# Performance work log

Hardware: AMD Instinct MI355X
Metric: run time of the kernel (lower is better)

The kernel has to match this reference:

```python
import jax, jax.numpy as jnp
import numpy as np

N = 100000      # nodes
E = 1600000     # edges
NODE_DIM = 128
HID = 128
L = 3           # num_layers
B = 512         # graphs in batch
EPS = 1e-5      # LayerNorm eps


def setup_inputs() -> dict:
    key = jax.random.key(0)
    ks = jax.random.split(key, 8)
    nodes = jax.random.normal(ks[0], (N, NODE_DIM), jnp.float32)
    edges = jax.random.randint(ks[1], (2, E), 0, N, dtype=jnp.int32)
    edge_types = jax.random.randint(ks[2], (E,), 0, 10, dtype=jnp.int32)
    batch_idx = jnp.sort(jax.random.randint(ks[3], (N,), 0, B, dtype=jnp.int32))
    w_in = jax.random.normal(ks[4], (NODE_DIM, HID), jnp.float32) / np.sqrt(NODE_DIM)
    b_in = jnp.zeros((HID,), jnp.float32)
    gcn_w = jax.random.normal(ks[5], (L, HID, HID), jnp.float32) / np.sqrt(HID)
    gcn_b = jnp.zeros((L, HID), jnp.float32)
    ln_g = jnp.ones((L, HID), jnp.float32)
    ln_b = jnp.zeros((L, HID), jnp.float32)
    return {"nodes": nodes, "edges": edges, "edge_types": edge_types,
            "batch_idx": batch_idx, "w_in": w_in, "b_in": b_in,
            "gcn_w": gcn_w, "gcn_b": gcn_b, "ln_g": ln_g, "ln_b": ln_b}


def _layer_norm(x, g, b):
    mu = jnp.mean(x, axis=-1, keepdims=True)
    var = jnp.mean(jnp.square(x - mu), axis=-1, keepdims=True)
    return (x - mu) * jax.lax.rsqrt(var + EPS) * g + b


def reference(nodes, edges, edge_types, batch_idx, w_in, b_in, gcn_w, gcn_b, ln_g, ln_b):
    src, dst = edges[0], edges[1]
    # GCN normalization with self-loops: deg = in-degree(A) + 1
    deg = jax.ops.segment_sum(jnp.ones((E,), nodes.dtype), dst, num_segments=N) + 1.0
    dinv_sqrt = jax.lax.rsqrt(deg)
    dinv = 1.0 / deg                       # self-loop norm = 1/deg_i
    enorm = dinv_sqrt[src] * dinv_sqrt[dst]

    x = nodes @ w_in + b_in                # input projection [N, HID]
    for i in range(L):
        res = x
        xw = x @ gcn_w[i]
        agg = jax.ops.segment_sum(xw[src] * enorm[:, None], dst, num_segments=N)
        x = agg + xw * dinv[:, None] + gcn_b[i]
        x = jax.nn.relu(_layer_norm(x, ln_g[i], ln_b[i]))
        # dropout is identity in eval mode
        if i > 0:
            x = x + res                    # residual only for i > 0

    # global mean pool per graph
    counts = jax.ops.segment_sum(jnp.ones((N,), x.dtype), batch_idx, num_segments=B)
    plan = jax.ops.segment_sum(x, batch_idx, num_segments=B) / jnp.maximum(counts, 1.0)[:, None]
    return x, plan
```

## Files before the change

kernel.cpp:

```cpp
#include <hip/hip_runtime.h>
#include <hip/hip_bf16.h>

typedef __attribute__((ext_vector_type(8))) short bf16x8;
typedef __attribute__((ext_vector_type(4))) float f32x4;
typedef __attribute__((ext_vector_type(2))) float f32x2;

#define K1_TILE 6144
#define NBCAP 4608
#define PAD 136

__device__ __forceinline__ unsigned short f2bf(float f) {
    union { unsigned int i; float f; } x; x.f = f;
    unsigned int r = (x.i + 0x7fffu + ((x.i >> 16) & 1u)) >> 16;
    return (unsigned short)r;
}
__device__ __forceinline__ float blo(unsigned int u) { return __uint_as_float(u << 16); }
__device__ __forceinline__ float bhi(unsigned int u) { return __uint_as_float(u & 0xffff0000u); }


__global__ __launch_bounds__(256) void bin2_k(const int* __restrict__ src,
                                              const int* __restrict__ dst,
                                              int* __restrict__ bucket_cursor,
                                              int* __restrict__ bins,
                                              int E, int NB) {
    __shared__ int hist[512];
    __shared__ int lbase[513];
    __shared__ int gdiff[512];
    __shared__ int wsum[4];
    __shared__ int stage[K1_TILE];
    int tid = threadIdx.x;
    int base = blockIdx.x * K1_TILE;
    int cnt = min(K1_TILE, E - base);

    hist[tid] = 0; hist[tid + 256] = 0;
    __syncthreads();
    for (int i = tid; i < cnt; i += 256) atomicAdd(&hist[dst[base + i] >> 8], 1);
    __syncthreads();

    int h0 = hist[2 * tid], h1 = hist[2 * tid + 1];
    int v = h0 + h1;
    int lane = tid & 63, wid = tid >> 6;
    int s = v;
#pragma unroll
    for (int o = 1; o < 64; o <<= 1) { int n = __shfl_up(s, o); if (lane >= o) s += n; }
    if (lane == 63) wsum[wid] = s;
    __syncthreads();
    if (tid == 0) { int r = 0; for (int w = 0; w < 4; ++w) { int t2 = wsum[w]; wsum[w] = r; r += t2; } }
    __syncthreads();
    int lb0 = s + wsum[wid] - v;
    int lb1 = lb0 + h0;
    int b0 = 2 * tid, b1 = 2 * tid + 1;
    int gb0 = 0, gb1 = 0;
    if (h0 > 0 && b0 < NB) gb0 = atomicAdd(&bucket_cursor[b0], h0);
    if (h1 > 0 && b1 < NB) gb1 = atomicAdd(&bucket_cursor[b1], h1);
    __syncthreads();
    hist[b0] = lb0; hist[b1] = lb1;
    lbase[b0] = lb0; lbase[b1] = lb1;
    gdiff[b0] = gb0 - lb0; gdiff[b1] = gb1 - lb1;
    if (tid == 0) lbase[512] = cnt;
    __syncthreads();

    for (int i = tid; i < cnt; i += 256) {
        int sv = src[base + i], dv = dst[base + i];
        int pos = atomicAdd(&hist[dv >> 8], 1);
        stage[pos] = ((dv & 255) << 24) | sv;
    }
    __syncthreads();

    for (int i = tid; i < cnt; i += 256) {
        int lo = 0, hi = 512;
        while (lo + 1 < hi) { int mid = (lo + hi) >> 1; if (lbase[mid] <= i) lo = mid; else hi = mid; }
        int p = gdiff[lo] + i;
        if (p < NBCAP) bins[(size_t)lo * NBCAP + p] = stage[i];
    }
}


__global__ __launch_bounds__(256) void bucket_scan_k(const int* __restrict__ bucket_cursor,
                                                     int* __restrict__ bucket_base, int NB) {
    __shared__ int wsum[4];
    int tid = threadIdx.x;
    int h0 = (2 * tid < NB) ? min(bucket_cursor[2 * tid], NBCAP) : 0;
    int h1 = (2 * tid + 1 < NB) ? min(bucket_cursor[2 * tid + 1], NBCAP) : 0;
    int v = h0 + h1;
    int lane = tid & 63, wid = tid >> 6;
    int s = v;
#pragma unroll
    for (int o = 1; o < 64; o <<= 1) { int n = __shfl_up(s, o); if (lane >= o) s += n; }
    if (lane == 63) wsum[wid] = s;
    __syncthreads();
    if (tid == 0) { int r = 0; for (int w = 0; w < 4; ++w) { int t2 = wsum[w]; wsum[w] = r; r += t2; } }
    __syncthreads();
    int excl = s + wsum[wid] - v;
    if (2 * tid < NB) bucket_base[2 * tid] = excl;
    if (2 * tid + 1 < NB) bucket_base[2 * tid + 1] = excl + h0;
}


__global__ __launch_bounds__(256) void csr_build_k(const int* __restrict__ bins,
                                                   const int* __restrict__ bucket_cursor,
                                                   const int* __restrict__ bucket_base,
                                                   int* __restrict__ csr_src,
                                                   int* __restrict__ row_start,
                                                   float* __restrict__ dinv_sqrt,
                                                   float* __restrict__ dinv,
                                                   int N) {
    __shared__ int counts[256];
    __shared__ int cursor[256];
    __shared__ int wsum[4];
    __shared__ int lcsr[NBCAP];
    int b = blockIdx.x, tid = threadIdx.x;
    int cnt = min(bucket_cursor[b], NBCAP);
    int cbase = bucket_base[b];
    const int* my = bins + (size_t)b * NBCAP;

    counts[tid] = 0;
    __syncthreads();
    for (int i = tid; i < cnt; i += 256) atomicAdd(&counts[((unsigned)my[i]) >> 24], 1);
    __syncthreads();

    int v = counts[tid];
    int lane = tid & 63, wid = tid >> 6;
    int s = v;
#pragma unroll
    for (int o = 1; o < 64; o <<= 1) { int n = __shfl_up(s, o); if (lane >= o) s += n; }
    if (lane == 63) wsum[wid] = s;
    __syncthreads();
    if (tid == 0) { int r = 0; for (int w = 0; w < 4; ++w) { int t2 = wsum[w]; wsum[w] = r; r += t2; } }
    __syncthreads();
    int excl = s + wsum[wid] - v;

    int node = b * 256 + tid;
    if (node <= N) row_start[node] = cbase + excl;
    if (node < N) {
        float dg = (float)v + 1.0f;
        dinv_sqrt[node] = rsqrtf(dg);
        dinv[node] = 1.0f / dg;
    }
    cursor[tid] = excl;
    __syncthreads();

    for (int i = tid; i < cnt; i += 256) {
        int e = my[i];
        int pos = atomicAdd(&cursor[((unsigned)e) >> 24], 1);
        lcsr[pos] = e & 0xffffff;
    }
    __syncthreads();
    for (int i = tid; i < cnt; i += 256) csr_src[cbase + i] = lcsr[i];
}


__global__ __launch_bounds__(256) void pack_w_k(const float* __restrict__ w_in,
                                                const float* __restrict__ gcn_w,
                                                unsigned short* __restrict__ Wp) {
    int t = blockIdx.x * 256 + threadIdx.x;
    if (t >= 8192) return;
    int mat = t >> 11;
    int kb = (t >> 9) & 3;
    int ct = (t >> 6) & 7;
    int lane = t & 63;
    int q = lane >> 4, c = lane & 15;
    const float* W = (mat == 0) ? w_in : (gcn_w + (size_t)(mat - 1) * 16384);
    unsigned short o[8];
#pragma unroll
    for (int j = 0; j < 8; ++j)
        o[j] = f2bf(W[(size_t)(kb * 32 + q * 8 + j) * 128 + ct * 16 + c]);
    unsigned short* dstp = Wp + ((size_t)t) * 8;
#pragma unroll
    for (int j = 0; j < 8; ++j) dstp[j] = o[j];
}


__global__ __launch_bounds__(256) void proj_k(const float* __restrict__ A,
                                              const unsigned short* __restrict__ Wp,
                                              const float* __restrict__ bias,
                                              unsigned short* __restrict__ Cb,
                                              int M) {
    __shared__ unsigned short stage[64 * 128];
    int wid = threadIdx.x >> 6, lane = threadIdx.x & 63;
    int blk0 = blockIdx.x * 64;
    int r0 = blk0 + wid * 16;
    int q = lane >> 4, c = lane & 15;
    int ar = min(r0 + c, M - 1);

    f32x4 acc[8];
#pragma unroll
    for (int ct = 0; ct < 8; ++ct) acc[ct] = (f32x4){0.f, 0.f, 0.f, 0.f};

#pragma unroll
    for (int kb = 0; kb < 4; ++kb) {
        float4 f0 = *(const float4*)&A[(size_t)ar * 128 + kb * 32 + q * 8];
        float4 f1 = *(const float4*)&A[(size_t)ar * 128 + kb * 32 + q * 8 + 4];
        union { unsigned short u[8]; bf16x8 v; } af;
        af.u[0] = f2bf(f0.x); af.u[1] = f2bf(f0.y); af.u[2] = f2bf(f0.z); af.u[3] = f2bf(f0.w);
        af.u[4] = f2bf(f1.x); af.u[5] = f2bf(f1.y); af.u[6] = f2bf(f1.z); af.u[7] = f2bf(f1.w);
#pragma unroll
        for (int ct = 0; ct < 8; ++ct) {
            bf16x8 b = *(const bf16x8*)&Wp[(((size_t)(kb * 8 + ct)) * 64 + lane) * 8];
            acc[ct] = __builtin_amdgcn_mfma_f32_16x16x32_bf16(af.v, b, acc[ct], 0, 0, 0);
        }
    }

#pragma unroll
    for (int ct = 0; ct < 8; ++ct) {
        int col = ct * 16 + c;
        float bv = bias[col];
#pragma unroll
        for (int r = 0; r < 4; ++r)
            stage[(wid * 16 + q * 4 + r) * 128 + col] = f2bf(acc[ct][r] + bv);
    }
    __syncthreads();

    int tid = threadIdx.x;
#pragma unroll
    for (int i = 0; i < 4; ++i) {
        int k = tid + i * 256;
        int row = k >> 4, colc = (k & 15) * 8;
        int grow = blk0 + row;
        if (grow < M)
            *(uint4*)&Cb[(size_t)grow * 128 + colc] = *(const uint4*)&stage[row * 128 + colc];
    }
}


__device__ __forceinline__ void acc8(f32x2& a0, f32x2& a1, f32x2& a2, f32x2& a3,
                                     uint4 u, float w) {
    f32x2 w2 = {w, w};
    f32x2 p0 = {blo(u.x), bhi(u.x)};
    f32x2 p1 = {blo(u.y), bhi(u.y)};
    f32x2 p2 = {blo(u.z), bhi(u.z)};
    f32x2 p3 = {blo(u.w), bhi(u.w)};
    a0 += p0 * w2; a1 += p1 * w2; a2 += p2 * w2; a3 += p3 * w2;
}

__global__ __launch_bounds__(256) void aggemm_k(const unsigned short* __restrict__ xin,
                                                unsigned short* __restrict__ xout,
                                                float* __restrict__ xf32,
                                                const int* __restrict__ row_start,
                                                const int* __restrict__ csr_src,
                                                const float* __restrict__ dst_tbl,
                                                const float* __restrict__ dinv,
                                                const unsigned short* __restrict__ Wp,
                                                const float* __restrict__ bias,
                                                const float* __restrict__ g,
                                                const float* __restrict__ bb,
                                                int N, int residual, int write_f32) {
    __shared__ unsigned short stage[64 * PAD];
    int wid = threadIdx.x >> 6, lane = threadIdx.x & 63;
    int blk0 = blockIdx.x * 64;
    int nbase = blk0 + wid * 16;
    int grp = lane >> 4, sl = lane & 15;
    int c0 = sl * 8;

    int rsv = 0;
    if (lane < 17) rsv = row_start[min(nbase + lane, N)];

    for (int i = 0; i < 16; ++i) {
        int n = nbase + i;
        int beg = __shfl(rsv, i), end = __shfl(rsv, i + 1);
        if (n >= N) continue;
        int deg = end - beg;

        int pidx = 0; float pw = 0.f;
        if (lane < deg) {
            pidx = csr_src[beg + lane];
            pw = dst_tbl[pidx];
        }

        f32x2 a0 = {0.f, 0.f}, a1 = {0.f, 0.f}, a2 = {0.f, 0.f}, a3 = {0.f, 0.f};
        int dcap = min(deg, 64);
        for (int j = 0; j < dcap; j += 16) {
            int e0 = j + grp, e1 = e0 + 4, e2 = e0 + 8, e3 = e0 + 12;
            int s0 = __shfl(pidx, e0); float w0 = __shfl(pw, e0);
            int s1 = __shfl(pidx, e1); float w1 = __shfl(pw, e1);
            int s2 = __shfl(pidx, e2); float w2 = __shfl(pw, e2);
            int s3 = __shfl(pidx, e3); float w3 = __shfl(pw, e3);
            uint4 u0 = *(const uint4*)(xin + (s0 * 128 + c0));
            uint4 u1 = *(const uint4*)(xin + (s1 * 128 + c0));
            uint4 u2 = *(const uint4*)(xin + (s2 * 128 + c0));
            uint4 u3 = *(const uint4*)(xin + (s3 * 128 + c0));
            acc8(a0, a1, a2, a3, u0, w0);
            acc8(a0, a1, a2, a3, u1, w1);
            acc8(a0, a1, a2, a3, u2, w2);
            acc8(a0, a1, a2, a3, u3, w3);
        }
        for (int j = 64; j < deg; j += 8) {
            int ja = j + grp, jb = j + grp + 4;
            int sa = csr_src[beg + min(ja, deg - 1)];
            int sb = csr_src[beg + min(jb, deg - 1)];
            float wa = (ja < deg) ? dst_tbl[sa] : 0.f;
            float wb = (jb < deg) ? dst_tbl[sb] : 0.f;
            uint4 ua = *(const uint4*)(xin + (sa * 128 + c0));
            uint4 ub = *(const uint4*)(xin + (sb * 128 + c0));
            acc8(a0, a1, a2, a3, ua, wa);
            acc8(a0, a1, a2, a3, ub, wb);
        }

#pragma unroll
        for (int o = 16; o <= 32; o <<= 1) {
            a0.x += __shfl_xor(a0.x, o); a0.y += __shfl_xor(a0.y, o);
            a1.x += __shfl_xor(a1.x, o); a1.y += __shfl_xor(a1.y, o);
            a2.x += __shfl_xor(a2.x, o); a2.y += __shfl_xor(a2.y, o);
            a3.x += __shfl_xor(a3.x, o); a3.y += __shfl_xor(a3.y, o);
        }

        if (grp == 0) {
            float dsd = dst_tbl[n];
            float di = dinv[n];
            uint4 u = *(const uint4*)(xin + (n * 128 + c0));
            float y0 = a0.x * dsd + blo(u.x) * di;
            float y1 = a0.y * dsd + bhi(u.x) * di;
            float y2 = a1.x * dsd + blo(u.y) * di;
            float y3 = a1.y * dsd + bhi(u.y) * di;
            float y4 = a2.x * dsd + blo(u.z) * di;
            float y5 = a2.y * dsd + bhi(u.z) * di;
            float y6 = a3.x * dsd + blo(u.w) * di;
            float y7 = a3.y * dsd + bhi(u.w) * di;
            union { unsigned short us[8]; uint4 qv; } o;
            o.us[0] = f2bf(y0); o.us[1] = f2bf(y1); o.us[2] = f2bf(y2); o.us[3] = f2bf(y3);
            o.us[4] = f2bf(y4); o.us[5] = f2bf(y5); o.us[6] = f2bf(y6); o.us[7] = f2bf(y7);
            *(uint4*)&stage[(wid * 16 + i) * PAD + c0] = o.qv;
        }
    }
    __syncthreads();

    int q = lane >> 4, c = lane & 15;

    f32x4 acc[8];
#pragma unroll
    for (int ct = 0; ct < 8; ++ct) acc[ct] = (f32x4){0.f, 0.f, 0.f, 0.f};

#pragma unroll
    for (int kb = 0; kb < 4; ++kb) {
        bf16x8 a = *(const bf16x8*)&stage[(wid * 16 + c) * PAD + kb * 32 + q * 8];
#pragma unroll
        for (int ct = 0; ct < 8; ++ct) {
            bf16x8 b = *(const bf16x8*)&Wp[(((size_t)(kb * 8 + ct)) * 64 + lane) * 8];
            acc[ct] = __builtin_amdgcn_mfma_f32_16x16x32_bf16(a, b, acc[ct], 0, 0, 0);
        }
    }

    float v[8][4];
#pragma unroll
    for (int ct = 0; ct < 8; ++ct) {
        float bv = bias[ct * 16 + c];
#pragma unroll
        for (int r = 0; r < 4; ++r) v[ct][r] = acc[ct][r] + bv;
    }

    float mu[4], rs[4];
#pragma unroll
    for (int r = 0; r < 4; ++r) {
        float s = 0.f;
#pragma unroll
        for (int ct = 0; ct < 8; ++ct) s += v[ct][r];
        s += __shfl_xor(s, 1); s += __shfl_xor(s, 2);
        s += __shfl_xor(s, 4); s += __shfl_xor(s, 8);
        mu[r] = s * (1.0f / 128.0f);
    }
#pragma unroll
    for (int r = 0; r < 4; ++r) {
        float s = 0.f;
#pragma unroll
        for (int ct = 0; ct < 8; ++ct) { float d = v[ct][r] - mu[r]; s += d * d; }
        s += __shfl_xor(s, 1); s += __shfl_xor(s, 2);
        s += __shfl_xor(s, 4); s += __shfl_xor(s, 8);
        rs[r] = rsqrtf(s * (1.0f / 128.0f) + 1e-5f);
    }

#pragma unroll
    for (int ct = 0; ct < 8; ++ct) {
        int col = ct * 16 + c;
        float gamma = g[col], beta = bb[col];
#pragma unroll
        for (int r = 0; r < 4; ++r) {
            float y = fmaxf((v[ct][r] - mu[r]) * rs[r] * gamma + beta, 0.f);
            stage[(wid * 16 + q * 4 + r) * PAD + col] = f2bf(y);
        }
    }
    __syncthreads();

    int tid = threadIdx.x;
#pragma unroll
    for (int i = 0; i < 4; ++i) {
        int k = tid + i * 256;
        int row = k >> 4, colc = (k & 15) * 8;
        int grow = blk0 + row;
        if (grow >= N) continue;
        uint4 sv = *(const uint4*)&stage[row * PAD + colc];
        float y0 = blo(sv.x), y1 = bhi(sv.x), y2 = blo(sv.y), y3 = bhi(sv.y);
        float y4 = blo(sv.z), y5 = bhi(sv.z), y6 = blo(sv.w), y7 = bhi(sv.w);
        if (residual) {
            uint4 rv = *(const uint4*)&xin[(size_t)grow * 128 + colc];
            y0 += blo(rv.x); y1 += bhi(rv.x); y2 += blo(rv.y); y3 += bhi(rv.y);
            y4 += blo(rv.z); y5 += bhi(rv.z); y6 += blo(rv.w); y7 += bhi(rv.w);
        }
        union { unsigned short u[8]; uint4 qv; } o;
        o.u[0] = f2bf(y0); o.u[1] = f2bf(y1); o.u[2] = f2bf(y2); o.u[3] = f2bf(y3);
        o.u[4] = f2bf(y4); o.u[5] = f2bf(y5); o.u[6] = f2bf(y6); o.u[7] = f2bf(y7);
        *(uint4*)&xout[(size_t)grow * 128 + colc] = o.qv;
        if (write_f32) {
            *(float4*)&xf32[(size_t)grow * 128 + colc] = make_float4(y0, y1, y2, y3);
            *(float4*)&xf32[(size_t)grow * 128 + colc + 4] = make_float4(y4, y5, y6, y7);
        }
    }
}


__global__ __launch_bounds__(256) void bounds_k(const int* __restrict__ bidx,
                                                int* __restrict__ gstart, int N, int B) {
    int i = blockIdx.x * 256 + threadIdx.x;
    if (i > N) return;
    int cur = (i < N) ? bidx[i] : B;
    int prev = (i == 0) ? -1 : bidx[i - 1];
    for (int b = prev + 1; b <= cur; ++b) gstart[b] = i;
}

__global__ __launch_bounds__(256) void pool_k(const unsigned short* __restrict__ x,
                                              const int* __restrict__ gstart,
                                              float* __restrict__ plan) {
    __shared__ float red[8 * 128];
    int b = blockIdx.x, t = threadIdx.x;
    int cg = (t & 31) * 4;
    int h = t >> 5;
    int s = gstart[b], e = gstart[b + 1];
    float acc0 = 0.f, acc1 = 0.f, acc2 = 0.f, acc3 = 0.f;
    for (int i = s + h; i < e; i += 8) {
        uint2 u = *(const uint2*)&x[(size_t)i * 128 + cg];
        acc0 += blo(u.x); acc1 += bhi(u.x); acc2 += blo(u.y); acc3 += bhi(u.y);
    }
    red[h * 128 + cg] = acc0; red[h * 128 + cg + 1] = acc1;
    red[h * 128 + cg + 2] = acc2; red[h * 128 + cg + 3] = acc3;
    __syncthreads();
    if (h == 0) {
#pragma unroll
        for (int k = 1; k < 8; ++k) {
            acc0 += red[k * 128 + cg];     acc1 += red[k * 128 + cg + 1];
            acc2 += red[k * 128 + cg + 2]; acc3 += red[k * 128 + cg + 3];
        }
        float inv = 1.0f / (float)max(e - s, 1);
        *(float4*)&plan[(size_t)b * 128 + cg] = make_float4(acc0 * inv, acc1 * inv,
                                                            acc2 * inv, acc3 * inv);
    }
}


extern "C" void kernel_launch(void* const* d_in, const int* in_sizes, int n_in,
                              void* d_out, int out_size, void* d_ws, size_t ws_size,
                              hipStream_t stream) {
    const float* nodes     = (const float*)d_in[0];
    const int*   edges     = (const int*)d_in[1];
    const int*   batch_idx = (const int*)d_in[3];
    const float* w_in      = (const float*)d_in[4];
    const float* b_in      = (const float*)d_in[5];
    const float* gcn_w     = (const float*)d_in[6];
    const float* gcn_b     = (const float*)d_in[7];
    const float* ln_g      = (const float*)d_in[8];
    const float* ln_b      = (const float*)d_in[9];

    const int N = in_sizes[0] / 128;
    const int E = in_sizes[1] / 2;
    const int B = out_size / 128 - N;
    const int* src = edges;
    const int* dst = edges + E;
    const int NB = (N + 256) / 256;

    float* xbuf = (float*)d_out;
    float* plan = xbuf + (size_t)N * 128;

    unsigned short* xa   = (unsigned short*)d_ws;
    unsigned short* xb   = xa + (size_t)N * 128;
    unsigned short* Wp   = xb + (size_t)N * 128;
    int* bins            = (int*)(Wp + 4 * 16384);
    int* bucket_cursor   = bins + (size_t)NB * NBCAP;
    int* bucket_base     = bucket_cursor + NB;
    int* csr_src         = bucket_base + NB;
    int* row_start       = csr_src + E;
    float* dinv_sqrt     = (float*)(row_start + N + 1);
    float* dinv          = dinv_sqrt + N;
    int* gstart          = (int*)(dinv + N);

    hipMemsetAsync(bucket_cursor, 0, sizeof(int) * NB, stream);

    bin2_k<<<(E + K1_TILE - 1) / K1_TILE, 256, 0, stream>>>(src, dst, bucket_cursor, bins, E, NB);
    bucket_scan_k<<<1, 256, 0, stream>>>(bucket_cursor, bucket_base, NB);
    csr_build_k<<<NB, 256, 0, stream>>>(bins, bucket_cursor, bucket_base,
                                        csr_src, row_start, dinv_sqrt, dinv, N);

    pack_w_k<<<32, 256, 0, stream>>>(w_in, gcn_w, Wp);

    proj_k<<<(N + 63) / 64, 256, 0, stream>>>(nodes, Wp, b_in, xa, N);

    const int nblk = (N + 63) / 64;
    for (int l = 0; l < 3; ++l) {
        unsigned short* xin  = (l & 1) ? xb : xa;
        unsigned short* xout = (l & 1) ? xa : xb;
        aggemm_k<<<nblk, 256, 0, stream>>>(xin, xout, xbuf, row_start, csr_src,
                                           dinv_sqrt, dinv,
                                           Wp + (size_t)(l + 1) * 16384,
                                           gcn_b + (size_t)l * 128,
                                           ln_g + (size_t)l * 128,
                                           ln_b + (size_t)l * 128, N,
                                           l > 0 ? 1 : 0, l == 2 ? 1 : 0);
    }

    bounds_k<<<(N + 1 + 255) / 256, 256, 0, stream>>>(batch_idx, gstart, N, B);
    pool_k<<<B, 256, 0, stream>>>(xb, gstart, plan);
}
```

Measured before the change: 457.1 us.

## Replace bucketed binning CSR build with global atomic count, scan, scatter

Replaces the two-level bucket binning CSR construction, which staged edges in shared memory and sorted within 256-node buckets, with a plain global pipeline. The new path counts in-degrees with global atomics, runs a three-kernel prefix scan, and scatters source ids with per-node atomic cursors. This drops the NBCAP overflow cap and the extra bins buffer. In exchange it relies on random global atomics and uncoalesced scatter writes, and edge order within a row becomes nondeterministic, which can change floating-point summation order.

Measured after the change: 591.5 us. 1.29x slower.

```diff
diff --git a/kernel.cpp b/kernel.cpp
--- a/kernel.cpp
+++ b/kernel.cpp
@@ -5,8 +5,6 @@
 typedef __attribute__((ext_vector_type(4))) float f32x4;
 typedef __attribute__((ext_vector_type(2))) float f32x2;
 
-#define K1_TILE 6144
-#define NBCAP 4608
 #define PAD 136
 
 __device__ __forceinline__ unsigned short f2bf(float f) {
@@ -18,135 +16,87 @@
 __device__ __forceinline__ float bhi(unsigned int u) { return __uint_as_float(u & 0xffff0000u); }
 
 
-__global__ __launch_bounds__(256) void bin2_k(const int* __restrict__ src,
-                                              const int* __restrict__ dst,
-                                              int* __restrict__ bucket_cursor,
-                                              int* __restrict__ bins,
-                                              int E, int NB) {
-    __shared__ int hist[512];
-    __shared__ int lbase[513];
-    __shared__ int gdiff[512];
+__global__ __launch_bounds__(256) void count_k(const int* __restrict__ dst,
+                                               int* __restrict__ deg, int E) {
+    int i = blockIdx.x * 256 + threadIdx.x;
+    if (i < E) atomicAdd(&deg[dst[i]], 1);
+}
+
+__global__ __launch_bounds__(256) void scanA_k(const int* __restrict__ deg,
+                                               int* __restrict__ row_start,
+                                               int* __restrict__ bsum, int N) {
     __shared__ int wsum[4];
-    __shared__ int stage[K1_TILE];
-    int tid = threadIdx.x;
-    int base = blockIdx.x * K1_TILE;
-    int cnt = min(K1_TILE, E - base);
-
-    hist[tid] = 0; hist[tid + 256] = 0;
-    __syncthreads();
-    for (int i = tid; i < cnt; i += 256) atomicAdd(&hist[dst[base + i] >> 8], 1);
-    __syncthreads();
-
-    int h0 = hist[2 * tid], h1 = hist[2 * tid + 1];
-    int v = h0 + h1;
-    int lane = tid & 63, wid = tid >> 6;
+    int b = blockIdx.x, t = threadIdx.x;
+    int base = b * 1024 + t * 4;
+    int d0 = (base + 0 < N) ? deg[base + 0] : 0;
+    int d1 = (base + 1 < N) ? deg[base + 1] : 0;
+    int d2 = (base + 2 < N) ? deg[base + 2] : 0;
+    int d3 = (base + 3 < N) ? deg[base + 3] : 0;
+    int v = d0 + d1 + d2 + d3;
+    int lane = t & 63, wid = t >> 6;
     int s = v;
 #pragma unroll
     for (int o = 1; o < 64; o <<= 1) { int n = __shfl_up(s, o); if (lane >= o) s += n; }
     if (lane == 63) wsum[wid] = s;
     __syncthreads();
-    if (tid == 0) { int r = 0; for (int w = 0; w < 4; ++w) { int t2 = wsum[w]; wsum[w] = r; r += t2; } }
-    __syncthreads();
-    int lb0 = s + wsum[wid] - v;
-    int lb1 = lb0 + h0;
-    int b0 = 2 * tid, b1 = 2 * tid + 1;
-    int gb0 = 0, gb1 = 0;
-    if (h0 > 0 && b0 < NB) gb0 = atomicAdd(&bucket_cursor[b0], h0);
-    if (h1 > 0 && b1 < NB) gb1 = atomicAdd(&bucket_cursor[b1], h1);
-    __syncthreads();
-    hist[b0] = lb0; hist[b1] = lb1;
-    lbase[b0] = lb0; lbase[b1] = lb1;
-    gdiff[b0] = gb0 - lb0; gdiff[b1] = gb1 - lb1;
-    if (tid == 0) lbase[512] = cnt;
-    __syncthreads();
-
-    for (int i = tid; i < cnt; i += 256) {
-        int sv = src[base + i], dv = dst[base + i];
-        int pos = atomicAdd(&hist[dv >> 8], 1);
-        stage[pos] = ((dv & 255) << 24) | sv;
-    }
-    __syncthreads();
-
-    for (int i = tid; i < cnt; i += 256) {
-        int lo = 0, hi = 512;
-        while (lo + 1 < hi) { int mid = (lo + hi) >> 1; if (lbase[mid] <= i) lo = mid; else hi = mid; }
-        int p = gdiff[lo] + i;
-        if (p < NBCAP) bins[(size_t)lo * NBCAP + p] = stage[i];
-    }
-}
-
-
-__global__ __launch_bounds__(256) void bucket_scan_k(const int* __restrict__ bucket_cursor,
-                                                     int* __restrict__ bucket_base, int NB) {
+    if (t == 0) { int r = 0; for (int w = 0; w < 4; ++w) { int t2 = wsum[w]; wsum[w] = r; r += t2; } }
+    __syncthreads();
+    int excl = s + wsum[wid] - v;
+    if (base + 0 < N) row_start[base + 0] = excl;
+    if (base + 1 < N) row_start[base + 1] = excl + d0;
+    if (base + 2 < N) row_start[base + 2] = excl + d0 + d1;
+    if (base + 3 < N) row_start[base + 3] = excl + d0 + d1 + d2;
+    if (t == 255) bsum[b] = excl + v;
+}
+
+__global__ __launch_bounds__(256) void scanB_k(int* __restrict__ bsum, int nblk) {
     __shared__ int wsum[4];
-    int tid = threadIdx.x;
-    int h0 = (2 * tid < NB) ? min(bucket_cursor[2 * tid], NBCAP) : 0;
-    int h1 = (2 * tid + 1 < NB) ? min(bucket_cursor[2 * tid + 1], NBCAP) : 0;
+    int t = threadIdx.x;
+    int h0 = (2 * t < nblk) ? bsum[2 * t] : 0;
+    int h1 = (2 * t + 1 < nblk) ? bsum[2 * t + 1] : 0;
     int v = h0 + h1;
-    int lane = tid & 63, wid = tid >> 6;
+    int lane = t & 63, wid = t >> 6;
     int s = v;
 #pragma unroll
     for (int o = 1; o < 64; o <<= 1) { int n = __shfl_up(s, o); if (lane >= o) s += n; }
     if (lane == 63) wsum[wid] = s;
     __syncthreads();
-    if (tid == 0) { int r = 0; for (int w = 0; w < 4; ++w) { int t2 = wsum[w]; wsum[w] = r; r += t2; } }
+    if (t == 0) { int r = 0; for (int w = 0; w < 4; ++w) { int t2 = wsum[w]; wsum[w] = r; r += t2; } }
     __syncthreads();
     int excl = s + wsum[wid] - v;
-    if (2 * tid < NB) bucket_base[2 * tid] = excl;
-    if (2 * tid + 1 < NB) bucket_base[2 * tid + 1] = excl + h0;
-}
-
-
-__global__ __launch_bounds__(256) void csr_build_k(const int* __restrict__ bins,
-                                                   const int* __restrict__ bucket_cursor,
-                                                   const int* __restrict__ bucket_base,
-                                                   int* __restrict__ csr_src,
-                                                   int* __restrict__ row_start,
-                                                   float* __restrict__ dinv_sqrt,
-                                                   float* __restrict__ dinv,
-                                                   int N) {
-    __shared__ int counts[256];
-    __shared__ int cursor[256];
-    __shared__ int wsum[4];
-    __shared__ int lcsr[NBCAP];
-    int b = blockIdx.x, tid = threadIdx.x;
-    int cnt = min(bucket_cursor[b], NBCAP);
-    int cbase = bucket_base[b];
-    const int* my = bins + (size_t)b * NBCAP;
-
-    counts[tid] = 0;
-    __syncthreads();
-    for (int i = tid; i < cnt; i += 256) atomicAdd(&counts[((unsigned)my[i]) >> 24], 1);
-    __syncthreads();
-
-    int v = counts[tid];
-    int lane = tid & 63, wid = tid >> 6;
-    int s = v;
-#pragma unroll
-    for (int o = 1; o < 64; o <<= 1) { int n = __shfl_up(s, o); if (lane >= o) s += n; }
-    if (lane == 63) wsum[wid] = s;
-    __syncthreads();
-    if (tid == 0) { int r = 0; for (int w = 0; w < 4; ++w) { int t2 = wsum[w]; wsum[w] = r; r += t2; } }
-    __syncthreads();
-    int excl = s + wsum[wid] - v;
-
-    int node = b * 256 + tid;
-    if (node <= N) row_start[node] = cbase + excl;
-    if (node < N) {
-        float dg = (float)v + 1.0f;
-        dinv_sqrt[node] = rsqrtf(dg);
-        dinv[node] = 1.0f / dg;
-    }
-    cursor[tid] = excl;
-    __syncthreads();
-
-    for (int i = tid; i < cnt; i += 256) {
-        int e = my[i];
-        int pos = atomicAdd(&cursor[((unsigned)e) >> 24], 1);
-        lcsr[pos] = e & 0xffffff;
-    }
-    __syncthreads();
-    for (int i = tid; i < cnt; i += 256) csr_src[cbase + i] = lcsr[i];
+    if (2 * t < nblk) bsum[2 * t] = excl;
+    if (2 * t + 1 < nblk) bsum[2 * t + 1] = excl + h0;
+}
+
+__global__ __launch_bounds__(256) void scanC_k(const int* __restrict__ deg,
+                                               const int* __restrict__ bsum,
+                                               int* __restrict__ row_start,
+                                               int* __restrict__ cursor,
+                                               float* __restrict__ dinv_sqrt,
+                                               float* __restrict__ dinv,
+                                               int N, int E) {
+    int i = blockIdx.x * 256 + threadIdx.x;
+    if (i < N) {
+        int rs = row_start[i] + bsum[i >> 10];
+        row_start[i] = rs;
+        cursor[i] = rs;
+        float dg = (float)deg[i] + 1.0f;
+        dinv_sqrt[i] = rsqrtf(dg);
+        dinv[i] = 1.0f / dg;
+    } else if (i == N) {
+        row_start[N] = E;
+    }
+}
+
+__global__ __launch_bounds__(256) void scatter_k(const int* __restrict__ src,
+                                                 const int* __restrict__ dst,
+                                                 int* __restrict__ cursor,
+                                                 int* __restrict__ csr_src, int E) {
+    int i = blockIdx.x * 256 + threadIdx.x;
+    if (i >= E) return;
+    int d = dst[i];
+    int pos = atomicAdd(&cursor[d], 1);
+    csr_src[pos] = src[i];
 }
 
 
@@ -463,7 +413,7 @@
     const int B = out_size / 128 - N;
     const int* src = edges;
     const int* dst = edges + E;
-    const int NB = (N + 256) / 256;
+    const int NSCAN = (N + 1023) / 1024;
 
     float* xbuf = (float*)d_out;
     float* plan = xbuf + (size_t)N * 128;
@@ -471,21 +421,24 @@
     unsigned short* xa   = (unsigned short*)d_ws;
     unsigned short* xb   = xa + (size_t)N * 128;
     unsigned short* Wp   = xb + (size_t)N * 128;
-    int* bins            = (int*)(Wp + 4 * 16384);
-    int* bucket_cursor   = bins + (size_t)NB * NBCAP;
-    int* bucket_base     = bucket_cursor + NB;
-    int* csr_src         = bucket_base + NB;
+    int* csr_src         = (int*)(Wp + 4 * 16384);
     int* row_start       = csr_src + E;
-    float* dinv_sqrt     = (float*)(row_start + N + 1);
+    int* deg             = row_start + N + 1;
+    int* cursor          = deg + N;
+    int* bsum            = cursor + N;
+    float* dinv_sqrt     = (float*)(bsum + 512);
     float* dinv          = dinv_sqrt + N;
     int* gstart          = (int*)(dinv + N);
 
-    hipMemsetAsync(bucket_cursor, 0, sizeof(int) * NB, stream);
-
-    bin2_k<<<(E + K1_TILE - 1) / K1_TILE, 256, 0, stream>>>(src, dst, bucket_cursor, bins, E, NB);
-    bucket_scan_k<<<1, 256, 0, stream>>>(bucket_cursor, bucket_base, NB);
-    csr_build_k<<<NB, 256, 0, stream>>>(bins, bucket_cursor, bucket_base,
-                                        csr_src, row_start, dinv_sqrt, dinv, N);
+    hipMemsetAsync(deg, 0, sizeof(int) * N, stream);
+
+    const int eblk = (E + 255) / 256;
+    count_k<<<eblk, 256, 0, stream>>>(dst, deg, E);
+    scanA_k<<<NSCAN, 256, 0, stream>>>(deg, row_start, bsum, N);
+    scanB_k<<<1, 256, 0, stream>>>(bsum, NSCAN);
+    scanC_k<<<(N + 256) / 256, 256, 0, stream>>>(deg, bsum, row_start, cursor,
+                                                 dinv_sqrt, dinv, N, E);
+    scatter_k<<<eblk, 256, 0, stream>>>(src, dst, cursor, csr_src, E);
 
     pack_w_k<<<32, 256, 0, stream>>>(w_in, gcn_w, Wp);
 
```
